# Performance work log

Hardware: AMD Instinct MI355X
Metric: run time of the kernel (lower is better)

## Reference

```python
import jax, jax.numpy as jnp
import numpy as np

N_NODES = 100000
N_EDGES = 3200000
F_IN = 256
H1 = 128   # growth_rate * bn_size
H2 = 32    # growth_rate
BN_EPS = 1e-5


def _gin_bn_relu(x, edge_index, Wa, ba, Wb, bb, gamma, beta):
    # GINConv (eps=0): h_i = MLP(x_i + sum_{j in N(i)} x_j)
    src, dst = edge_index[0], edge_index[1]
    agg = jax.ops.segment_sum(x[src], dst, num_segments=x.shape[0])  # [N, F]
    h = x + agg
    # nn1: Linear -> ReLU -> Linear
    h = jnp.maximum(h @ Wa + ba, 0.0)
    h = h @ Wb + bb
    # BatchNorm1d (training-mode batch stats over nodes)
    mean = h.mean(axis=0)
    var = h.var(axis=0)  # biased, matches torch BN normalization
    h = (h - mean) * jax.lax.rsqrt(var + BN_EPS) * gamma + beta
    return jnp.maximum(h, 0.0)


def setup_inputs() -> dict:
    key = jax.random.key(0)
    ks = jax.random.split(key, 12)
    x = jax.random.normal(ks[0], (N_NODES, F_IN), dtype=jnp.float32)
    edge_index = jax.random.randint(ks[1], (2, N_EDGES), 0, N_NODES, dtype=jnp.int64)

    def lin(k, fin, fout):
        s = 1.0 / np.sqrt(fin)
        return jax.random.uniform(k, (fin, fout), jnp.float32, -s, s)

    return {
        "x": x,
        "edge_index": edge_index,
        "W1a": lin(ks[2], F_IN, H1), "b1a": jnp.zeros((H1,), jnp.float32),
        "W1b": lin(ks[3], H1, H1),   "b1b": jnp.zeros((H1,), jnp.float32),
        "g1": jnp.ones((H1,), jnp.float32), "be1": jnp.zeros((H1,), jnp.float32),
        "W2a": lin(ks[4], H1, H2),   "b2a": jnp.zeros((H2,), jnp.float32),
        "W2b": lin(ks[5], H2, H2),   "b2b": jnp.zeros((H2,), jnp.float32),
        "g2": jnp.ones((H2,), jnp.float32), "be2": jnp.zeros((H2,), jnp.float32),
    }


def reference(x, edge_index, W1a, b1a, W1b, b1b, g1, be1,
              W2a, b2a, W2b, b2b, g2, be2):
    # data.x is a single tensor -> [x]; torch.cat([x], 1) == x (concat is a no-op)
    h = _gin_bn_relu(x, edge_index, W1a, b1a, W1b, b1b, g1, be1)   # [N, 128]
    h = _gin_bn_relu(h, edge_index, W2a, b2a, W2b, b2b, g2, be2)   # [N, 32]
    return h
```

## Files before the change

### kernel.cpp

```cpp
#include <hip/hip_runtime.h>

#define F_IN 256
#define H1 128
#define H2 32
#define BN_EPS 1e-5f
#define BSHIFT 9
#define BCAP 32768
#define NSHARD 8

typedef short bf16x8 __attribute__((ext_vector_type(8)));
typedef float f32x4 __attribute__((ext_vector_type(4)));

__device__ __forceinline__ ushort f2bf(float f) {
    uint u = __float_as_uint(f);
    return (ushort)((u + 0x7FFFu + ((u >> 16) & 1u)) >> 16);
}
__device__ __forceinline__ float bf2f(ushort h) {
    return __uint_as_float((uint)h << 16);
}
__device__ __forceinline__ uint pack2(float a, float b) {
    return (uint)f2bf(a) | ((uint)f2bf(b) << 16);
}
__device__ __forceinline__ void unpack2(uint u, float& a, float& b) {
    a = __uint_as_float(u << 16);
    b = __uint_as_float(u & 0xFFFF0000u);
}

__global__ void detect_k(const int* __restrict__ eb, int* __restrict__ flag) {
    __shared__ int nz;
    if (threadIdx.x == 0) nz = 0;
    __syncthreads();
    if (eb[2 * threadIdx.x + 1] != 0) atomicAdd(&nz, 1);
    __syncthreads();
    if (threadIdx.x == 0) flag[0] = (nz == 0) ? 1 : 0;
}

__device__ __forceinline__ int clampN(int v, int N) {
    return v < 0 ? 0 : (v >= N ? N - 1 : v);
}

__global__ __launch_bounds__(256) void binA_k(const int* __restrict__ eb,
                                              const int* __restrict__ flag,
                                              int E, int N, int NBUCK,
                                              int* __restrict__ bucket_cursor,
                                              uint* __restrict__ rec) {
    __shared__ int lcnt[256];
    __shared__ int lbase[256];
    __shared__ uint lrec[4096];
    __shared__ ushort lbk[4096];
    __shared__ ushort lrk[4096];
    const int tid = threadIdx.x;
    const int is64 = flag[0];
    const int cbase = blockIdx.x * 4096;
    const int cnum = min(4096, E - cbase);
    if (cnum <= 0) return;
    for (int i = tid; i < NBUCK; i += 256) lcnt[i] = 0;
    __syncthreads();
    for (int i = tid; i < cnum; i += 256) {
        int e = cbase + i;
        int s = is64 ? eb[2 * e] : eb[e];
        int d = is64 ? eb[2 * (E + e)] : eb[E + e];
        s = clampN(s, N);
        d = clampN(d, N);
        int bk = d >> BSHIFT;
        int rk = atomicAdd(&lcnt[bk], 1);
        lrec[i] = (uint)s | ((uint)(d & 511) << 17);
        lbk[i] = (ushort)bk;
        lrk[i] = (ushort)rk;
    }
    __syncthreads();
    for (int i = tid; i < NBUCK; i += 256)
        lbase[i] = atomicAdd(&bucket_cursor[i], lcnt[i]);
    __syncthreads();
    for (int i = tid; i < cnum; i += 256) {
        int bk = lbk[i];
        int pos = lbase[bk] + lrk[i];
        if (pos < BCAP) rec[(size_t)bk * BCAP + pos] = lrec[i];
    }
}

__global__ void bscan_k(const int* __restrict__ bucket_cursor, int NBUCK, int N,
                        int* __restrict__ ebase, int* __restrict__ row_start) {
    if (threadIdx.x == 0 && blockIdx.x == 0) {
        int acc = 0;
        for (int i = 0; i < NBUCK; ++i) {
            ebase[i] = acc;
            int c = bucket_cursor[i];
            acc += (c < BCAP) ? c : BCAP;
        }
        ebase[NBUCK] = acc;
        row_start[N] = acc;
    }
}

__global__ __launch_bounds__(256) void binB_k(const uint* __restrict__ rec,
                                              const int* __restrict__ bucket_cursor,
                                              const int* __restrict__ ebase,
                                              int N, int* __restrict__ row_start,
                                              int* __restrict__ esrc) {
    __shared__ int cntA[512];
    __shared__ int cntB[512];
    const int bk = blockIdx.x;
    const int tid = threadIdx.x;
    int cnt = bucket_cursor[bk];
    if (cnt > BCAP) cnt = BCAP;
    const uint* r = rec + (size_t)bk * BCAP;
    const int base = ebase[bk];
    for (int i = tid; i < 512; i += 256) cntA[i] = 0;
    __syncthreads();
    for (int i = tid; i < cnt; i += 256) atomicAdd(&cntA[r[i] >> 17], 1);
    __syncthreads();
    int* src = cntA;
    int* dst = cntB;
    for (int off = 1; off < 512; off <<= 1) {
        for (int i = tid; i < 512; i += 256)
            dst[i] = src[i] + (i >= off ? src[i - off] : 0);
        __syncthreads();
        int* t = src; src = dst; dst = t;
    }
    const int n0 = bk << BSHIFT;
    for (int i = tid; i < 512; i += 256) {
        int node = n0 + i;
        if (node < N) row_start[node] = base + (i ? src[i - 1] : 0);
    }
    for (int i = tid; i < 512; i += 256) dst[i] = 0;
    __syncthreads();
    for (int i = tid; i < cnt; i += 256) {
        uint rv = r[i];
        int dl = rv >> 17;
        int rank = atomicAdd(&dst[dl], 1);
        esrc[base + (dl ? src[dl - 1] : 0) + rank] = (int)(rv & 0x1FFFFu);
    }
}

__global__ void wcast_k(const float* __restrict__ W1a, const float* __restrict__ W1b,
                        const float* __restrict__ W2a, const float* __restrict__ W2b,
                        ushort* __restrict__ w1aT, ushort* __restrict__ w1bT,
                        ushort* __restrict__ w2aT, ushort* __restrict__ w2bT) {
    int idx = blockIdx.x * 256 + threadIdx.x;
    if (idx < 32768) {
        int k = idx >> 7, c = idx & 127;
        w1aT[c * 256 + k] = f2bf(W1a[idx]);
    } else if (idx < 49152) {
        int t = idx - 32768;
        int k = t >> 7, c = t & 127;
        w1bT[c * 128 + k] = f2bf(W1b[t]);
    } else if (idx < 53248) {
        int t = idx - 49152;
        int k = t >> 5, c = t & 31;
        w2aT[c * 128 + k] = f2bf(W2a[t]);
    } else if (idx < 54272) {
        int t = idx - 53248;
        int k = t >> 5, c = t & 31;
        w2bT[c * 32 + k] = f2bf(W2b[t]);
    }
}

template <int NC, bool BIAS, bool OUT_BF16, bool STATS, int NF>
__device__ __forceinline__ void gemm_epilogue(f32x4* acc, const float* bias,
                                              void* outv, int N, int row0,
                                              int lane, float* sums) {
    __shared__ float ssum[NC];
    __shared__ float ssq[NC];
    if (STATS) {
        if (threadIdx.x < NC) { ssum[threadIdx.x] = 0.f; ssq[threadIdx.x] = 0.f; }
        __syncthreads();
    }
    const int col0 = lane & 15;
    const int crow = row0 + (lane >> 4) * 4;
#pragma unroll
    for (int f = 0; f < NF; ++f) {
        const int c = f * 16 + col0;
        float bv = BIAS ? bias[c] : 0.f;
        float sv = 0.f, qv = 0.f;
#pragma unroll
        for (int j = 0; j < 4; ++j) {
            int rr = crow + j;
            if (rr < N) {
                float v = acc[f][j] + bv;
                if (OUT_BF16) ((ushort*)outv)[(size_t)rr * NC + c] = f2bf(v);
                else          ((float*)outv)[(size_t)rr * NC + c] = v;
                if (STATS) { sv += v; qv += v * v; }
            }
        }
        if (STATS) {
            sv += __shfl_xor(sv, 16); sv += __shfl_xor(sv, 32);
            qv += __shfl_xor(qv, 16); qv += __shfl_xor(qv, 32);
            if ((lane >> 4) == 0) {
                atomicAdd(&ssum[c], sv);
                atomicAdd(&ssq[c], qv);
            }
        }
    }
    if (STATS) {
        __syncthreads();
        if (threadIdx.x < NC) {
            float* sh = sums + (blockIdx.x & (NSHARD - 1)) * 2 * NC;
            atomicAdd(&sh[threadIdx.x], ssum[threadIdx.x]);
            atomicAdd(&sh[NC + threadIdx.x], ssq[threadIdx.x]);
        }
    }
}

template <int K, int NC, bool BIAS, bool OUT_BF16, bool STATS>
__global__ __launch_bounds__(256) void gemm_mfma_k(const ushort* __restrict__ A,
                                                   const ushort* __restrict__ WT,
                                                   const float* __restrict__ bias,
                                                   void* __restrict__ outv, int N,
                                                   float* __restrict__ sums) {
    constexpr int NF = NC / 16;
    const int lane = threadIdx.x & 63;
    const int wave = threadIdx.x >> 6;
    const int row0 = blockIdx.x * 64 + wave * 16;
    const int col = lane & 15;
    const int k0 = (lane >> 4) * 8;
    int arow = row0 + col;
    if (arow >= N) arow = N - 1;

    f32x4 acc[NF];
#pragma unroll
    for (int f = 0; f < NF; ++f) acc[f] = (f32x4){0.f, 0.f, 0.f, 0.f};
#pragma unroll
    for (int kc = 0; kc < K; kc += 32) {
        bf16x8 af = *(const bf16x8*)&A[(size_t)arow * K + kc + k0];
#pragma unroll
        for (int f = 0; f < NF; ++f) {
            bf16x8 bf = *(const bf16x8*)&WT[(size_t)(f * 16 + col) * K + kc + k0];
            acc[f] = __builtin_amdgcn_mfma_f32_16x16x32_bf16(af, bf, acc[f], 0, 0, 0);
        }
    }
    gemm_epilogue<NC, BIAS, OUT_BF16, STATS, NF>(acc, bias, outv, N, row0, lane, sums);
}

template <int K, int NC, bool OUT_BF16>
__global__ __launch_bounds__(256) void gemm_mfma_f32a_k(const float* __restrict__ Af,
                                                        const ushort* __restrict__ WT,
                                                        void* __restrict__ outv, int N) {
    constexpr int NF = NC / 16;
    const int lane = threadIdx.x & 63;
    const int wave = threadIdx.x >> 6;
    const int row0 = blockIdx.x * 64 + wave * 16;
    const int col = lane & 15;
    const int k0 = (lane >> 4) * 8;
    int arow = row0 + col;
    if (arow >= N) arow = N - 1;

    f32x4 acc[NF];
#pragma unroll
    for (int f = 0; f < NF; ++f) acc[f] = (f32x4){0.f, 0.f, 0.f, 0.f};
#pragma unroll
    for (int kc = 0; kc < K; kc += 32) {
        const float* ap = &Af[(size_t)arow * K + kc + k0];
        float4 p = *(const float4*)ap;
        float4 q = *(const float4*)(ap + 4);
        bf16x8 af;
        af[0] = (short)f2bf(p.x); af[1] = (short)f2bf(p.y);
        af[2] = (short)f2bf(p.z); af[3] = (short)f2bf(p.w);
        af[4] = (short)f2bf(q.x); af[5] = (short)f2bf(q.y);
        af[6] = (short)f2bf(q.z); af[7] = (short)f2bf(q.w);
#pragma unroll
        for (int f = 0; f < NF; ++f) {
            bf16x8 bf = *(const bf16x8*)&WT[(size_t)(f * 16 + col) * K + kc + k0];
            acc[f] = __builtin_amdgcn_mfma_f32_16x16x32_bf16(af, bf, acc[f], 0, 0, 0);
        }
    }
    gemm_epilogue<NC, false, OUT_BF16, false, NF>(acc, nullptr, outv, N, row0, lane, nullptr);
}

template <int K, int NC, bool OUT_BF16>
__global__ __launch_bounds__(256) void gemm_mfma_bnA_k(const ushort* __restrict__ U,
                                                       const ushort* __restrict__ WT,
                                                       const float* __restrict__ sc,
                                                       const float* __restrict__ sh,
                                                       void* __restrict__ outv, int N) {
    constexpr int NF = NC / 16;
    const int lane = threadIdx.x & 63;
    const int wave = threadIdx.x >> 6;
    const int row0 = blockIdx.x * 64 + wave * 16;
    const int col = lane & 15;
    const int k0 = (lane >> 4) * 8;
    int arow = row0 + col;
    if (arow >= N) arow = N - 1;

    f32x4 acc[NF];
#pragma unroll
    for (int f = 0; f < NF; ++f) acc[f] = (f32x4){0.f, 0.f, 0.f, 0.f};
#pragma unroll
    for (int kc = 0; kc < K; kc += 32) {
        bf16x8 raw = *(const bf16x8*)&U[(size_t)arow * K + kc + k0];
        float4 c0 = *(const float4*)&sc[kc + k0];
        float4 c1 = *(const float4*)&sc[kc + k0 + 4];
        float4 h0 = *(const float4*)&sh[kc + k0];
        float4 h1 = *(const float4*)&sh[kc + k0 + 4];
        bf16x8 af;
        af[0] = (short)f2bf(fmaxf(bf2f((ushort)raw[0]) * c0.x + h0.x, 0.f));
        af[1] = (short)f2bf(fmaxf(bf2f((ushort)raw[1]) * c0.y + h0.y, 0.f));
        af[2] = (short)f2bf(fmaxf(bf2f((ushort)raw[2]) * c0.z + h0.z, 0.f));
        af[3] = (short)f2bf(fmaxf(bf2f((ushort)raw[3]) * c0.w + h0.w, 0.f));
        af[4] = (short)f2bf(fmaxf(bf2f((ushort)raw[4]) * c1.x + h1.x, 0.f));
        af[5] = (short)f2bf(fmaxf(bf2f((ushort)raw[5]) * c1.y + h1.y, 0.f));
        af[6] = (short)f2bf(fmaxf(bf2f((ushort)raw[6]) * c1.z + h1.z, 0.f));
        af[7] = (short)f2bf(fmaxf(bf2f((ushort)raw[7]) * c1.w + h1.w, 0.f));
#pragma unroll
        for (int f = 0; f < NF; ++f) {
            bf16x8 bf = *(const bf16x8*)&WT[(size_t)(f * 16 + col) * K + kc + k0];
            acc[f] = __builtin_amdgcn_mfma_f32_16x16x32_bf16(af, bf, acc[f], 0, 0, 0);
        }
    }
    gemm_epilogue<NC, false, OUT_BF16, false, NF>(acc, nullptr, outv, N, row0, lane, nullptr);
}

__global__ void agg_f128b_k(const ushort* __restrict__ T, const int* __restrict__ row_start,
                            const int* __restrict__ esrc, const float* __restrict__ bias,
                            ushort* __restrict__ out, int N) {
    const int hw = (blockIdx.x << 3) | (threadIdx.x >> 5);
    const int lane = threadIdx.x & 31;
    if (hw >= N) return;
    const uint2* T2 = (const uint2*)T;
    uint2 sv = T2[(size_t)hw * 32 + lane];
    float a0, a1, a2, a3;
    unpack2(sv.x, a0, a1);
    unpack2(sv.y, a2, a3);
    int p = row_start[hw];
    const int pe = row_start[hw + 1];
    for (; p + 3 < pe; p += 4) {
        int s0 = esrc[p], s1 = esrc[p + 1], s2 = esrc[p + 2], s3 = esrc[p + 3];
        uint2 v0 = T2[(size_t)s0 * 32 + lane];
        uint2 v1 = T2[(size_t)s1 * 32 + lane];
        uint2 v2 = T2[(size_t)s2 * 32 + lane];
        uint2 v3 = T2[(size_t)s3 * 32 + lane];
        float x0, x1, x2, x3;
        unpack2(v0.x, x0, x1); unpack2(v0.y, x2, x3);
        a0 += x0; a1 += x1; a2 += x2; a3 += x3;
        unpack2(v1.x, x0, x1); unpack2(v1.y, x2, x3);
        a0 += x0; a1 += x1; a2 += x2; a3 += x3;
        unpack2(v2.x, x0, x1); unpack2(v2.y, x2, x3);
        a0 += x0; a1 += x1; a2 += x2; a3 += x3;
        unpack2(v3.x, x0, x1); unpack2(v3.y, x2, x3);
        a0 += x0; a1 += x1; a2 += x2; a3 += x3;
    }
    for (; p < pe; ++p) {
        uint2 v = T2[(size_t)esrc[p] * 32 + lane];
        float x0, x1, x2, x3;
        unpack2(v.x, x0, x1); unpack2(v.y, x2, x3);
        a0 += x0; a1 += x1; a2 += x2; a3 += x3;
    }
    const float4 b = ((const float4*)bias)[lane];
    a0 = fmaxf(a0 + b.x, 0.f);
    a1 = fmaxf(a1 + b.y, 0.f);
    a2 = fmaxf(a2 + b.z, 0.f);
    a3 = fmaxf(a3 + b.w, 0.f);
    ((uint2*)out)[(size_t)hw * 32 + lane] = make_uint2(pack2(a0, a1), pack2(a2, a3));
}

__global__ void agg_f32b_k(const ushort* __restrict__ T, const int* __restrict__ row_start,
                           const int* __restrict__ esrc, const float* __restrict__ bias,
                           ushort* __restrict__ out, int N) {
    const int wid = (blockIdx.x << 2) | (threadIdx.x >> 6);
    const int lane = threadIdx.x & 63;
    const int g = lane >> 3, l8 = lane & 7;
    if (wid >= N) return;
    const uint2* T2 = (const uint2*)T;
    float a0 = 0.f, a1 = 0.f, a2 = 0.f, a3 = 0.f;
    const int p0 = row_start[wid];
    const int pe = row_start[wid + 1];
    for (int p = p0 + g; p < pe; p += 8) {
        uint2 v = T2[(size_t)esrc[p] * 8 + l8];
        float x0, x1, x2, x3;
        unpack2(v.x, x0, x1); unpack2(v.y, x2, x3);
        a0 += x0; a1 += x1; a2 += x2; a3 += x3;
    }
#pragma unroll
    for (int off = 8; off < 64; off <<= 1) {
        a0 += __shfl_xor(a0, off);
        a1 += __shfl_xor(a1, off);
        a2 += __shfl_xor(a2, off);
        a3 += __shfl_xor(a3, off);
    }
    if (g == 0) {
        uint2 sv = T2[(size_t)wid * 8 + l8];
        float s0, s1, s2, s3;
        unpack2(sv.x, s0, s1); unpack2(sv.y, s2, s3);
        const float4 b = ((const float4*)bias)[l8];
        a0 = fmaxf(a0 + s0 + b.x, 0.f);
        a1 = fmaxf(a1 + s1 + b.y, 0.f);
        a2 = fmaxf(a2 + s2 + b.z, 0.f);
        a3 = fmaxf(a3 + s3 + b.w, 0.f);
        ((uint2*)out)[(size_t)wid * 8 + l8] = make_uint2(pack2(a0, a1), pack2(a2, a3));
    }
}

template <int F>
__global__ void finalize_k(const float* __restrict__ sums, const float* __restrict__ g,
                           const float* __restrict__ be, int N,
                           float* __restrict__ scale, float* __restrict__ shift) {
    const int c = threadIdx.x;
    if (c < F) {
        float s = 0.f, q = 0.f;
        for (int sh = 0; sh < NSHARD; ++sh) {
            s += sums[sh * 2 * F + c];
            q += sums[sh * 2 * F + F + c];
        }
        float inv_n = 1.f / (float)N;
        float mean = s * inv_n;
        float var = q * inv_n - mean * mean;
        float sc = g[c] * rsqrtf(var + BN_EPS);
        scale[c] = sc;
        shift[c] = be[c] - mean * sc;
    }
}

template <int F>
__global__ void bnapply_k(const float* __restrict__ U, const float* __restrict__ scale,
                          const float* __restrict__ shift, float* __restrict__ out, int total4) {
    const float4* U4 = (const float4*)U;
    const float4* S4 = (const float4*)scale;
    const float4* H4 = (const float4*)shift;
    float4* O4 = (float4*)out;
    const int stride = gridDim.x * blockDim.x;
    for (int i = blockIdx.x * blockDim.x + threadIdx.x; i < total4; i += stride) {
        int c4 = i % (F / 4);
        float4 u = U4[i], sc = S4[c4], sh = H4[c4];
        float4 o;
        o.x = fmaxf(u.x * sc.x + sh.x, 0.f);
        o.y = fmaxf(u.y * sc.y + sh.y, 0.f);
        o.z = fmaxf(u.z * sc.z + sh.z, 0.f);
        o.w = fmaxf(u.w * sc.w + sh.w, 0.f);
        O4[i] = o;
    }
}

extern "C" void kernel_launch(void* const* d_in, const int* in_sizes, int n_in,
                              void* d_out, int out_size, void* d_ws, size_t ws_size,
                              hipStream_t stream) {
    const float* x   = (const float*)d_in[0];
    const int*   eb  = (const int*)d_in[1];
    const float* W1a = (const float*)d_in[2];
    const float* b1a = (const float*)d_in[3];
    const float* W1b = (const float*)d_in[4];
    const float* b1b = (const float*)d_in[5];
    const float* g1  = (const float*)d_in[6];
    const float* be1 = (const float*)d_in[7];
    const float* W2a = (const float*)d_in[8];
    const float* b2a = (const float*)d_in[9];
    const float* W2b = (const float*)d_in[10];
    const float* b2b = (const float*)d_in[11];
    const float* g2  = (const float*)d_in[12];
    const float* be2 = (const float*)d_in[13];
    float* out = (float*)d_out;

    const int N = in_sizes[0] / F_IN;
    const int E = in_sizes[1] / 2;
    const int NBUCK = (N + 511) >> BSHIFT;

    char* w = (char*)d_ws;
    size_t off = 0;
    auto alloc = [&](size_t bytes) -> void* {
        void* p = w + off;
        off = (off + bytes + 255) & ~(size_t)255;
        return p;
    };
    ushort* B0 = (ushort*)alloc((size_t)N * H1 * 2);
    ushort* B1 = (ushort*)alloc((size_t)N * H1 * 2);
    char*   B2 = (char*)alloc((size_t)N * H1 * 4);
    ushort* u1b = (ushort*)B2;
    float*  u2  = (float*)B2;

    int* row_start = (int*)alloc((size_t)(N + 1) * 4);
    int* esrc      = (int*)alloc((size_t)E * 4);
    uint* rec      = (uint*)alloc((size_t)NBUCK * BCAP * 4);
    int* bucket_cursor = (int*)alloc(512 * 4);
    int* ebase     = (int*)alloc(513 * 4);
    int* flag      = (int*)alloc(256);
    ushort* w1aT = (ushort*)alloc(F_IN * H1 * 2);
    ushort* w1bT = (ushort*)alloc(H1 * H1 * 2);
    ushort* w2aT = (ushort*)alloc(H1 * H2 * 2);
    ushort* w2bT = (ushort*)alloc(H2 * H2 * 2);
    float* sums1 = (float*)alloc(NSHARD * 2 * H1 * 4);
    float* sc1   = (float*)alloc(H1 * 4);
    float* sh1   = (float*)alloc(H1 * 4);
    float* sums2 = (float*)alloc(NSHARD * 2 * H2 * 4);
    float* sc2   = (float*)alloc(H2 * 4);
    float* sh2   = (float*)alloc(H2 * 4);

    hipMemsetAsync(bucket_cursor, 0, 512 * 4, stream);
    hipMemsetAsync(sums1, 0, NSHARD * 2 * H1 * 4, stream);
    hipMemsetAsync(sums2, 0, NSHARD * 2 * H2 * 4, stream);

    wcast_k<<<213, 256, 0, stream>>>(W1a, W1b, W2a, W2b, w1aT, w1bT, w2aT, w2bT);

    detect_k<<<1, 128, 0, stream>>>(eb, flag);
    binA_k<<<(E + 4095) / 4096, 256, 0, stream>>>(eb, flag, E, N, NBUCK, bucket_cursor, rec);
    bscan_k<<<1, 64, 0, stream>>>(bucket_cursor, NBUCK, N, ebase, row_start);
    binB_k<<<NBUCK, 256, 0, stream>>>(rec, bucket_cursor, ebase, N, row_start, esrc);

    const int gemm_grid = (N + 63) / 64;

    gemm_mfma_f32a_k<F_IN, H1, true><<<gemm_grid, 256, 0, stream>>>(x, w1aT, B1, N);
    agg_f128b_k<<<(N + 7) / 8, 256, 0, stream>>>(B1, row_start, esrc, b1a, B0, N);
    gemm_mfma_k<H1, H1, true, true, true><<<gemm_grid, 256, 0, stream>>>(B0, w1bT, b1b, u1b, N, sums1);
    finalize_k<H1><<<1, 128, 0, stream>>>(sums1, g1, be1, N, sc1, sh1);
    gemm_mfma_bnA_k<H1, H2, true><<<gemm_grid, 256, 0, stream>>>(u1b, w2aT, sc1, sh1, B1, N);

    agg_f32b_k<<<(N + 3) / 4, 256, 0, stream>>>(B1, row_start, esrc, b2a, B0, N);
    gemm_mfma_k<H2, H2, true, false, true><<<gemm_grid, 256, 0, stream>>>(B0, w2bT, b2b, u2, N, sums2);
    finalize_k<H2><<<1, 32, 0, stream>>>(sums2, g2, be2, N, sc2, sh2);
    bnapply_k<H2><<<3125, 256, 0, stream>>>(u2, sc2, sh2, out, N * H2 / 4);
}
```

Before: 426.8 us.

## Merge setup kernels, co-schedule edge binning with first GEMM, fold BN finalize

Replaces the three memsets, the weight cast, the int64 detection, the bucket scan and both BN finalize kernels with fused variants. Bucket zeroing now happens inside the weight-cast kernel. Edge binning and the first x@W1a GEMM run as disjoint block ranges of one launch so they overlap. binB computes its bucket base with a per-block reduction instead of a serial scan kernel, and buckets are halved to 256 nodes with smaller chunks. The aim is fewer launches and serial tiny kernels, at the cost of every block redundantly recomputing the BN scale and shift, and a per-chunk int64 check based on sampled entries.

```diff
diff --git a/kernel.cpp b/kernel.cpp
--- a/kernel.cpp
+++ b/kernel.cpp
@@ -4,8 +4,9 @@
 #define H1 128
 #define H2 32
 #define BN_EPS 1e-5f
-#define BSHIFT 9
-#define BCAP 32768
+#define BSHIFT 8
+#define BCAP 16384
+#define CHUNK 2048
 #define NSHARD 8
 
 typedef short bf16x8 __attribute__((ext_vector_type(8)));
@@ -25,119 +26,25 @@
     a = __uint_as_float(u << 16);
     b = __uint_as_float(u & 0xFFFF0000u);
 }
-
-__global__ void detect_k(const int* __restrict__ eb, int* __restrict__ flag) {
-    __shared__ int nz;
-    if (threadIdx.x == 0) nz = 0;
-    __syncthreads();
-    if (eb[2 * threadIdx.x + 1] != 0) atomicAdd(&nz, 1);
-    __syncthreads();
-    if (threadIdx.x == 0) flag[0] = (nz == 0) ? 1 : 0;
-}
-
 __device__ __forceinline__ int clampN(int v, int N) {
     return v < 0 ? 0 : (v >= N ? N - 1 : v);
 }
 
-__global__ __launch_bounds__(256) void binA_k(const int* __restrict__ eb,
-                                              const int* __restrict__ flag,
-                                              int E, int N, int NBUCK,
-                                              int* __restrict__ bucket_cursor,
-                                              uint* __restrict__ rec) {
-    __shared__ int lcnt[256];
-    __shared__ int lbase[256];
-    __shared__ uint lrec[4096];
-    __shared__ ushort lbk[4096];
-    __shared__ ushort lrk[4096];
+__global__ __launch_bounds__(256) void super0_k(
+    const float* __restrict__ W1a, const float* __restrict__ W1b,
+    const float* __restrict__ W2a, const float* __restrict__ W2b,
+    ushort* __restrict__ w1aT, ushort* __restrict__ w1bT,
+    ushort* __restrict__ w2aT, ushort* __restrict__ w2bT,
+    int* __restrict__ bucket_cursor, float* __restrict__ sums1,
+    float* __restrict__ sums2) {
     const int tid = threadIdx.x;
-    const int is64 = flag[0];
-    const int cbase = blockIdx.x * 4096;
-    const int cnum = min(4096, E - cbase);
-    if (cnum <= 0) return;
-    for (int i = tid; i < NBUCK; i += 256) lcnt[i] = 0;
-    __syncthreads();
-    for (int i = tid; i < cnum; i += 256) {
-        int e = cbase + i;
-        int s = is64 ? eb[2 * e] : eb[e];
-        int d = is64 ? eb[2 * (E + e)] : eb[E + e];
-        s = clampN(s, N);
-        d = clampN(d, N);
-        int bk = d >> BSHIFT;
-        int rk = atomicAdd(&lcnt[bk], 1);
-        lrec[i] = (uint)s | ((uint)(d & 511) << 17);
-        lbk[i] = (ushort)bk;
-        lrk[i] = (ushort)rk;
-    }
-    __syncthreads();
-    for (int i = tid; i < NBUCK; i += 256)
-        lbase[i] = atomicAdd(&bucket_cursor[i], lcnt[i]);
-    __syncthreads();
-    for (int i = tid; i < cnum; i += 256) {
-        int bk = lbk[i];
-        int pos = lbase[bk] + lrk[i];
-        if (pos < BCAP) rec[(size_t)bk * BCAP + pos] = lrec[i];
-    }
-}
-
-__global__ void bscan_k(const int* __restrict__ bucket_cursor, int NBUCK, int N,
-                        int* __restrict__ ebase, int* __restrict__ row_start) {
-    if (threadIdx.x == 0 && blockIdx.x == 0) {
-        int acc = 0;
-        for (int i = 0; i < NBUCK; ++i) {
-            ebase[i] = acc;
-            int c = bucket_cursor[i];
-            acc += (c < BCAP) ? c : BCAP;
-        }
-        ebase[NBUCK] = acc;
-        row_start[N] = acc;
-    }
-}
-
-__global__ __launch_bounds__(256) void binB_k(const uint* __restrict__ rec,
-                                              const int* __restrict__ bucket_cursor,
-                                              const int* __restrict__ ebase,
-                                              int N, int* __restrict__ row_start,
-                                              int* __restrict__ esrc) {
-    __shared__ int cntA[512];
-    __shared__ int cntB[512];
-    const int bk = blockIdx.x;
-    const int tid = threadIdx.x;
-    int cnt = bucket_cursor[bk];
-    if (cnt > BCAP) cnt = BCAP;
-    const uint* r = rec + (size_t)bk * BCAP;
-    const int base = ebase[bk];
-    for (int i = tid; i < 512; i += 256) cntA[i] = 0;
-    __syncthreads();
-    for (int i = tid; i < cnt; i += 256) atomicAdd(&cntA[r[i] >> 17], 1);
-    __syncthreads();
-    int* src = cntA;
-    int* dst = cntB;
-    for (int off = 1; off < 512; off <<= 1) {
-        for (int i = tid; i < 512; i += 256)
-            dst[i] = src[i] + (i >= off ? src[i - off] : 0);
-        __syncthreads();
-        int* t = src; src = dst; dst = t;
-    }
-    const int n0 = bk << BSHIFT;
-    for (int i = tid; i < 512; i += 256) {
-        int node = n0 + i;
-        if (node < N) row_start[node] = base + (i ? src[i - 1] : 0);
-    }
-    for (int i = tid; i < 512; i += 256) dst[i] = 0;
-    __syncthreads();
-    for (int i = tid; i < cnt; i += 256) {
-        uint rv = r[i];
-        int dl = rv >> 17;
-        int rank = atomicAdd(&dst[dl], 1);
-        esrc[base + (dl ? src[dl - 1] : 0) + rank] = (int)(rv & 0x1FFFFu);
-    }
-}
-
-__global__ void wcast_k(const float* __restrict__ W1a, const float* __restrict__ W1b,
-                        const float* __restrict__ W2a, const float* __restrict__ W2b,
-                        ushort* __restrict__ w1aT, ushort* __restrict__ w1bT,
-                        ushort* __restrict__ w2aT, ushort* __restrict__ w2bT) {
-    int idx = blockIdx.x * 256 + threadIdx.x;
+    if (blockIdx.x == 212) {
+        for (int i = tid; i < 512; i += 256) bucket_cursor[i] = 0;
+        for (int i = tid; i < NSHARD * 2 * H1; i += 256) sums1[i] = 0.f;
+        for (int i = tid; i < NSHARD * 2 * H2; i += 256) sums2[i] = 0.f;
+        return;
+    }
+    int idx = blockIdx.x * 256 + tid;
     if (idx < 32768) {
         int k = idx >> 7, c = idx & 127;
         w1aT[c * 256 + k] = f2bf(W1a[idx]);
@@ -156,6 +63,161 @@
     }
 }
 
+__device__ __forceinline__ void binA_body(int bid, const int* __restrict__ eb,
+                                          int E, int N, int NBUCK,
+                                          int* __restrict__ bucket_cursor,
+                                          uint* __restrict__ rec) {
+    __shared__ int lcnt[512];
+    __shared__ int lbase[512];
+    __shared__ uint lrec[CHUNK];
+    __shared__ ushort lbk[CHUNK];
+    __shared__ ushort lrk[CHUNK];
+    __shared__ int nzf;
+    const int tid = threadIdx.x;
+    const int cbase = bid * CHUNK;
+    const int cnum = min(CHUNK, E - cbase);
+    if (cnum <= 0) return;
+    if (tid == 0) nzf = 0;
+    __syncthreads();
+    {
+        int i = tid * (CHUNK / 256);
+        if (i < cnum && eb[2 * (cbase + i) + 1] != 0) atomicAdd(&nzf, 1);
+    }
+    for (int i = tid; i < NBUCK; i += 256) lcnt[i] = 0;
+    __syncthreads();
+    const int is64 = (nzf == 0);
+    for (int i = tid; i < cnum; i += 256) {
+        int e = cbase + i;
+        int s = is64 ? eb[2 * e] : eb[e];
+        int d = is64 ? eb[2 * (E + e)] : eb[E + e];
+        s = clampN(s, N);
+        d = clampN(d, N);
+        int bk = d >> BSHIFT;
+        int rk = atomicAdd(&lcnt[bk], 1);
+        lrec[i] = (uint)s | ((uint)(d & 255) << 17);
+        lbk[i] = (ushort)bk;
+        lrk[i] = (ushort)rk;
+    }
+    __syncthreads();
+    for (int i = tid; i < NBUCK; i += 256)
+        lbase[i] = atomicAdd(&bucket_cursor[i], lcnt[i]);
+    __syncthreads();
+    for (int i = tid; i < cnum; i += 256) {
+        int bk = lbk[i];
+        int pos = lbase[bk] + lrk[i];
+        if (pos < BCAP) rec[(size_t)bk * BCAP + pos] = lrec[i];
+    }
+}
+
+__device__ __forceinline__ void gemm1_body(int bid, const float* __restrict__ Af,
+                                           const ushort* __restrict__ WT,
+                                           ushort* __restrict__ outb, int N) {
+    constexpr int K = F_IN, NC = H1, NF = NC / 16;
+    const int lane = threadIdx.x & 63;
+    const int wave = threadIdx.x >> 6;
+    const int row0 = bid * 64 + wave * 16;
+    const int col = lane & 15;
+    const int k0 = (lane >> 4) * 8;
+    int arow = row0 + col;
+    if (arow >= N) arow = N - 1;
+
+    f32x4 acc[NF];
+#pragma unroll
+    for (int f = 0; f < NF; ++f) acc[f] = (f32x4){0.f, 0.f, 0.f, 0.f};
+#pragma unroll
+    for (int kc = 0; kc < K; kc += 32) {
+        const float* ap = &Af[(size_t)arow * K + kc + k0];
+        float4 p = *(const float4*)ap;
+        float4 q = *(const float4*)(ap + 4);
+        bf16x8 af;
+        af[0] = (short)f2bf(p.x); af[1] = (short)f2bf(p.y);
+        af[2] = (short)f2bf(p.z); af[3] = (short)f2bf(p.w);
+        af[4] = (short)f2bf(q.x); af[5] = (short)f2bf(q.y);
+        af[6] = (short)f2bf(q.z); af[7] = (short)f2bf(q.w);
+#pragma unroll
+        for (int f = 0; f < NF; ++f) {
+            bf16x8 bf = *(const bf16x8*)&WT[(size_t)(f * 16 + col) * K + kc + k0];
+            acc[f] = __builtin_amdgcn_mfma_f32_16x16x32_bf16(af, bf, acc[f], 0, 0, 0);
+        }
+    }
+    const int crow = row0 + (lane >> 4) * 4;
+#pragma unroll
+    for (int f = 0; f < NF; ++f) {
+        const int c = f * 16 + col;
+#pragma unroll
+        for (int j = 0; j < 4; ++j) {
+            int rr = crow + j;
+            if (rr < N) outb[(size_t)rr * NC + c] = f2bf(acc[f][j]);
+        }
+    }
+}
+
+__global__ __launch_bounds__(256) void super1_k(
+    const int* __restrict__ eb, int E, int N, int NBUCK, int GB,
+    int* __restrict__ bucket_cursor, uint* __restrict__ rec,
+    const float* __restrict__ x, const ushort* __restrict__ w1aT,
+    ushort* __restrict__ t1b) {
+    if ((int)blockIdx.x < GB)
+        binA_body(blockIdx.x, eb, E, N, NBUCK, bucket_cursor, rec);
+    else
+        gemm1_body(blockIdx.x - GB, x, w1aT, t1b, N);
+}
+
+__global__ __launch_bounds__(256) void binB_k(const uint* __restrict__ rec,
+                                              const int* __restrict__ bucket_cursor,
+                                              int N, int NBUCK,
+                                              int* __restrict__ row_start,
+                                              int* __restrict__ esrc) {
+    __shared__ int cntA[256];
+    __shared__ int cntB[256];
+    __shared__ int red[256];
+    const int bk = blockIdx.x;
+    const int tid = threadIdx.x;
+    int part = 0;
+    for (int i = tid; i < bk; i += 256) {
+        int c = bucket_cursor[i];
+        part += (c < BCAP) ? c : BCAP;
+    }
+    red[tid] = part;
+    __syncthreads();
+    for (int s = 128; s > 0; s >>= 1) {
+        if (tid < s) red[tid] += red[tid + s];
+        __syncthreads();
+    }
+    const int base = red[0];
+    int cnt = bucket_cursor[bk];
+    if (cnt > BCAP) cnt = BCAP;
+    if (bk == NBUCK - 1 && tid == 0) row_start[N] = base + cnt;
+
+    const uint* r = rec + (size_t)bk * BCAP;
+    cntA[tid] = 0;
+    __syncthreads();
+    for (int i = tid; i < cnt; i += 256) atomicAdd(&cntA[r[i] >> 17], 1);
+    __syncthreads();
+    int* src = cntA;
+    int* dst = cntB;
+    for (int off = 1; off < 256; off <<= 1) {
+        int v = src[tid] + (tid >= off ? src[tid - off] : 0);
+        __syncthreads();
+        dst[tid] = v;
+        __syncthreads();
+        int* t = src; src = dst; dst = t;
+    }
+    const int n0 = bk << BSHIFT;
+    {
+        int node = n0 + tid;
+        if (node < N) row_start[node] = base + (tid ? src[tid - 1] : 0);
+    }
+    dst[tid] = 0;
+    __syncthreads();
+    for (int i = tid; i < cnt; i += 256) {
+        uint rv = r[i];
+        int dl = rv >> 17;
+        int rank = atomicAdd(&dst[dl], 1);
+        esrc[base + (dl ? src[dl - 1] : 0) + rank] = (int)(rv & 0x1FFFFu);
+    }
+}
+
 template <int NC, bool BIAS, bool OUT_BF16, bool STATS, int NF>
 __device__ __forceinline__ void gemm_epilogue(f32x4* acc, const float* bias,
                                               void* outv, int N, int row0,
@@ -233,12 +295,35 @@
 }
 
 template <int K, int NC, bool OUT_BF16>
-__global__ __launch_bounds__(256) void gemm_mfma_f32a_k(const float* __restrict__ Af,
-                                                        const ushort* __restrict__ WT,
-                                                        void* __restrict__ outv, int N) {
+__global__ __launch_bounds__(256) void gemm_mfma_bnA_k(const ushort* __restrict__ U,
+                                                       const ushort* __restrict__ WT,
+                                                       const float* __restrict__ sums,
+                                                       const float* __restrict__ g,
+                                                       const float* __restrict__ be,
+                                                       int Nbn,
+                                                       void* __restrict__ outv, int N) {
     constexpr int NF = NC / 16;
-    const int lane = threadIdx.x & 63;
-    const int wave = threadIdx.x >> 6;
+    __shared__ __align__(16) float lsc[K];
+    __shared__ __align__(16) float lsh[K];
+    const int tid = threadIdx.x;
+    if (tid < K) {
+        float s = 0.f, q = 0.f;
+#pragma unroll
+        for (int sh = 0; sh < NSHARD; ++sh) {
+            s += sums[sh * 2 * K + tid];
+            q += sums[sh * 2 * K + K + tid];
+        }
+        float inv_n = 1.f / (float)Nbn;
+        float mean = s * inv_n;
+        float var = q * inv_n - mean * mean;
+        float sc = g[tid] * rsqrtf(var + BN_EPS);
+        lsc[tid] = sc;
+        lsh[tid] = be[tid] - mean * sc;
+    }
+    __syncthreads();
+
+    const int lane = tid & 63;
+    const int wave = tid >> 6;
     const int row0 = blockIdx.x * 64 + wave * 16;
     const int col = lane & 15;
     const int k0 = (lane >> 4) * 8;
@@ -250,48 +335,11 @@
     for (int f = 0; f < NF; ++f) acc[f] = (f32x4){0.f, 0.f, 0.f, 0.f};
 #pragma unroll
     for (int kc = 0; kc < K; kc += 32) {
-        const float* ap = &Af[(size_t)arow * K + kc + k0];
-        float4 p = *(const float4*)ap;
-        float4 q = *(const float4*)(ap + 4);
-        bf16x8 af;
-        af[0] = (short)f2bf(p.x); af[1] = (short)f2bf(p.y);
-        af[2] = (short)f2bf(p.z); af[3] = (short)f2bf(p.w);
-        af[4] = (short)f2bf(q.x); af[5] = (short)f2bf(q.y);
-        af[6] = (short)f2bf(q.z); af[7] = (short)f2bf(q.w);
-#pragma unroll
-        for (int f = 0; f < NF; ++f) {
-            bf16x8 bf = *(const bf16x8*)&WT[(size_t)(f * 16 + col) * K + kc + k0];
-            acc[f] = __builtin_amdgcn_mfma_f32_16x16x32_bf16(af, bf, acc[f], 0, 0, 0);
-        }
-    }
-    gemm_epilogue<NC, false, OUT_BF16, false, NF>(acc, nullptr, outv, N, row0, lane, nullptr);
-}
-
-template <int K, int NC, bool OUT_BF16>
-__global__ __launch_bounds__(256) void gemm_mfma_bnA_k(const ushort* __restrict__ U,
-                                                       const ushort* __restrict__ WT,
-                                                       const float* __restrict__ sc,
-                                                       const float* __restrict__ sh,
-                                                       void* __restrict__ outv, int N) {
-    constexpr int NF = NC / 16;
-    const int lane = threadIdx.x & 63;
-    const int wave = threadIdx.x >> 6;
-    const int row0 = blockIdx.x * 64 + wave * 16;
-    const int col = lane & 15;
-    const int k0 = (lane >> 4) * 8;
-    int arow = row0 + col;
-    if (arow >= N) arow = N - 1;
-
-    f32x4 acc[NF];
-#pragma unroll
-    for (int f = 0; f < NF; ++f) acc[f] = (f32x4){0.f, 0.f, 0.f, 0.f};
-#pragma unroll
-    for (int kc = 0; kc < K; kc += 32) {
         bf16x8 raw = *(const bf16x8*)&U[(size_t)arow * K + kc + k0];
-        float4 c0 = *(const float4*)&sc[kc + k0];
-        float4 c1 = *(const float4*)&sc[kc + k0 + 4];
-        float4 h0 = *(const float4*)&sh[kc + k0];
-        float4 h1 = *(const float4*)&sh[kc + k0 + 4];
+        float4 c0 = *(const float4*)&lsc[kc + k0];
+        float4 c1 = *(const float4*)&lsc[kc + k0 + 4];
+        float4 h0 = *(const float4*)&lsh[kc + k0];
+        float4 h1 = *(const float4*)&lsh[kc + k0 + 4];
         bf16x8 af;
         af[0] = (short)f2bf(fmaxf(bf2f((ushort)raw[0]) * c0.x + h0.x, 0.f));
         af[1] = (short)f2bf(fmaxf(bf2f((ushort)raw[1]) * c0.y + h0.y, 0.f));
@@ -391,36 +439,35 @@
 }
 
 template <int F>
-__global__ void finalize_k(const float* __restrict__ sums, const float* __restrict__ g,
-                           const float* __restrict__ be, int N,
-                           float* __restrict__ scale, float* __restrict__ shift) {
-    const int c = threadIdx.x;
-    if (c < F) {
+__global__ void bnapply_fin_k(const float* __restrict__ U, const float* __restrict__ sums,
+                              const float* __restrict__ g, const float* __restrict__ be,
+                              int Nbn, float* __restrict__ out, int total4) {
+    __shared__ __align__(16) float lsc[F];
+    __shared__ __align__(16) float lsh[F];
+    const int tid = threadIdx.x;
+    if (tid < F) {
         float s = 0.f, q = 0.f;
+#pragma unroll
         for (int sh = 0; sh < NSHARD; ++sh) {
-            s += sums[sh * 2 * F + c];
-            q += sums[sh * 2 * F + F + c];
-        }
-        float inv_n = 1.f / (float)N;
+            s += sums[sh * 2 * F + tid];
+            q += sums[sh * 2 * F + F + tid];
+        }
+        float inv_n = 1.f / (float)Nbn;
         float mean = s * inv_n;
         float var = q * inv_n - mean * mean;
-        float sc = g[c] * rsqrtf(var + BN_EPS);
-        scale[c] = sc;
-        shift[c] = be[c] - mean * sc;
-    }
-}
-
-template <int F>
-__global__ void bnapply_k(const float* __restrict__ U, const float* __restrict__ scale,
-                          const float* __restrict__ shift, float* __restrict__ out, int total4) {
+        float sc = g[tid] * rsqrtf(var + BN_EPS);
+        lsc[tid] = sc;
+        lsh[tid] = be[tid] - mean * sc;
+    }
+    __syncthreads();
     const float4* U4 = (const float4*)U;
-    const float4* S4 = (const float4*)scale;
-    const float4* H4 = (const float4*)shift;
     float4* O4 = (float4*)out;
     const int stride = gridDim.x * blockDim.x;
-    for (int i = blockIdx.x * blockDim.x + threadIdx.x; i < total4; i += stride) {
-        int c4 = i % (F / 4);
-        float4 u = U4[i], sc = S4[c4], sh = H4[c4];
+    for (int i = blockIdx.x * blockDim.x + tid; i < total4; i += stride) {
+        int c4 = (i % (F / 4)) * 4;
+        float4 u = U4[i];
+        float4 sc = *(const float4*)&lsc[c4];
+        float4 sh = *(const float4*)&lsh[c4];
         float4 o;
         o.x = fmaxf(u.x * sc.x + sh.x, 0.f);
         o.y = fmaxf(u.y * sc.y + sh.y, 0.f);
@@ -451,7 +498,7 @@
 
     const int N = in_sizes[0] / F_IN;
     const int E = in_sizes[1] / 2;
-    const int NBUCK = (N + 511) >> BSHIFT;
+    const int NBUCK = (N + 255) >> BSHIFT;
 
     char* w = (char*)d_ws;
     size_t off = 0;
@@ -470,40 +517,25 @@
     int* esrc      = (int*)alloc((size_t)E * 4);
     uint* rec      = (uint*)alloc((size_t)NBUCK * BCAP * 4);
     int* bucket_cursor = (int*)alloc(512 * 4);
-    int* ebase     = (int*)alloc(513 * 4);
-    int* flag      = (int*)alloc(256);
     ushort* w1aT = (ushort*)alloc(F_IN * H1 * 2);
     ushort* w1bT = (ushort*)alloc(H1 * H1 * 2);
     ushort* w2aT = (ushort*)alloc(H1 * H2 * 2);
     ushort* w2bT = (ushort*)alloc(H2 * H2 * 2);
     float* sums1 = (float*)alloc(NSHARD * 2 * H1 * 4);
-    float* sc1   = (float*)alloc(H1 * 4);
-    float* sh1   = (float*)alloc(H1 * 4);
     float* sums2 = (float*)alloc(NSHARD * 2 * H2 * 4);
-    float* sc2   = (float*)alloc(H2 * 4);
-    float* sh2   = (float*)alloc(H2 * 4);
-
-    hipMemsetAsync(bucket_cursor, 0, 512 * 4, stream);
-    hipMemsetAsync(sums1, 0, NSHARD * 2 * H1 * 4, stream);
-    hipMemsetAsync(sums2, 0, NSHARD * 2 * H2 * 4, stream);
-
-    wcast_k<<<213, 256, 0, stream>>>(W1a, W1b, W2a, W2b, w1aT, w1bT, w2aT, w2bT);
-
-    detect_k<<<1, 128, 0, stream>>>(eb, flag);
-    binA_k<<<(E + 4095) / 4096, 256, 0, stream>>>(eb, flag, E, N, NBUCK, bucket_cursor, rec);
-    bscan_k<<<1, 64, 0, stream>>>(bucket_cursor, NBUCK, N, ebase, row_start);
-    binB_k<<<NBUCK, 256, 0, stream>>>(rec, bucket_cursor, ebase, N, row_start, esrc);
-
-    const int gemm_grid = (N + 63) / 64;
-
-    gemm_mfma_f32a_k<F_IN, H1, true><<<gemm_grid, 256, 0, stream>>>(x, w1aT, B1, N);
+
+    const int GB = (E + CHUNK - 1) / CHUNK;
+    const int G1 = (N + 63) / 64;
+
+    super0_k<<<213, 256, 0, stream>>>(W1a, W1b, W2a, W2b, w1aT, w1bT, w2aT, w2bT,
+                                      bucket_cursor, sums1, sums2);
+    super1_k<<<GB + G1, 256, 0, stream>>>(eb, E, N, NBUCK, GB, bucket_cursor, rec,
+                                          x, w1aT, B1);
+    binB_k<<<NBUCK, 256, 0, stream>>>(rec, bucket_cursor, N, NBUCK, row_start, esrc);
     agg_f128b_k<<<(N + 7) / 8, 256, 0, stream>>>(B1, row_start, esrc, b1a, B0, N);
-    gemm_mfma_k<H1, H1, true, true, true><<<gemm_grid, 256, 0, stream>>>(B0, w1bT, b1b, u1b, N, sums1);
-    finalize_k<H1><<<1, 128, 0, stream>>>(sums1, g1, be1, N, sc1, sh1);
-    gemm_mfma_bnA_k<H1, H2, true><<<gemm_grid, 256, 0, stream>>>(u1b, w2aT, sc1, sh1, B1, N);
-
+    gemm_mfma_k<H1, H1, true, true, true><<<G1, 256, 0, stream>>>(B0, w1bT, b1b, u1b, N, sums1);
+    gemm_mfma_bnA_k<H1, H2, true><<<G1, 256, 0, stream>>>(u1b, w2aT, sums1, g1, be1, N, B1, N);
     agg_f32b_k<<<(N + 3) / 4, 256, 0, stream>>>(B1, row_start, esrc, b2a, B0, N);
-    gemm_mfma_k<H2, H2, true, false, true><<<gemm_grid, 256, 0, stream>>>(B0, w2bT, b2b, u2, N, sums2);
-    finalize_k<H2><<<1, 32, 0, stream>>>(sums2, g2, be2, N, sc2, sh2);
-    bnapply_k<H2><<<3125, 256, 0, stream>>>(u2, sc2, sh2, out, N * H2 / 4);
-}
+    gemm_mfma_k<H2, H2, true, false, true><<<G1, 256, 0, stream>>>(B0, w2bT, b2b, u2, N, sums2);
+    bnapply_fin_k<H2><<<3125, 256, 0, stream>>>(u2, sums2, g2, be2, N, out, N * H2 / 4);
+}
```

New measurement: 387.2 us. 1.1x faster.
